# Kernel tuning notes

Measured on AMD Instinct MI355X. Metric: run time of the kernel, lower is better.

The kernel has to match this reference:

```python
import jax, jax.numpy as jnp
import numpy as np

B, C_IN, H, W = 8, 128, 64, 64
C_KEY, C_VAL, C_OUT = 64, 64, 128
BN_EPS = 1e-5
NORM_EPS = 1e-7


def setup_inputs() -> dict:
    key = jax.random.key(0)
    ks = jax.random.split(key, 8)
    s = 0.02
    return {
        "query_feature": jax.random.normal(ks[0], (B, C_IN, H, W), jnp.float32),
        "key_feature": jax.random.normal(ks[1], (B, C_IN, H, W), jnp.float32),
        "value_feature": jax.random.normal(ks[2], (B, C_IN, H, W), jnp.float32),
        "Wk": jax.random.normal(ks[3], (C_KEY, C_IN), jnp.float32) * s,  # shared f_key/f_query 1x1 conv
        "bk": jnp.zeros((C_KEY,), jnp.float32),
        "gamma": jnp.ones((C_KEY,), jnp.float32),   # BatchNorm2d weight
        "beta": jnp.zeros((C_KEY,), jnp.float32),   # BatchNorm2d bias
        "Wv": jax.random.normal(ks[4], (C_VAL, C_IN), jnp.float32) * s,
        "bv": jnp.zeros((C_VAL,), jnp.float32),
        "Ww": jax.random.normal(ks[5], (C_OUT, C_VAL), jnp.float32) * s,  # zero-init in original; random for nontrivial output
        "bw": jnp.zeros((C_OUT,), jnp.float32),
    }


def _conv1x1(x, w, b):
    # x: [B,C,H,W], w: [O,C] -> [B,O,H,W]
    return jnp.einsum('bchw,oc->bohw', x, w) + b[None, :, None, None]


def _bn_train(y, gamma, beta):
    # BatchNorm2d in train mode: batch stats over (B,H,W) per channel
    m = y.mean(axis=(0, 2, 3), keepdims=True)
    v = y.var(axis=(0, 2, 3), keepdims=True)
    return (y - m) * jax.lax.rsqrt(v + BN_EPS) * gamma[None, :, None, None] + beta[None, :, None, None]


def reference(query_feature, key_feature, value_feature, Wk, bk, gamma, beta, Wv, bv, Ww, bw):
    b, _, h, w = query_feature.shape
    n = h * w

    def f_key(x):
        return _bn_train(_conv1x1(x, Wk, bk), gamma, beta)

    # query: [B,N,Ck], key: [B,Ck,N], value: [B,N,Cv]
    q = f_key(query_feature).reshape(b, C_KEY, n).transpose(0, 2, 1)
    k = f_key(key_feature).reshape(b, C_KEY, n)
    v = _conv1x1(value_feature, Wv, bv).reshape(b, C_VAL, n).transpose(0, 2, 1)

    # L2-normalize over channel dim (cosine similarity)
    q = q / (jnp.linalg.norm(q, axis=2, keepdims=True) + NORM_EPS)
    k = k / (jnp.linalg.norm(k, axis=1, keepdims=True) + NORM_EPS)

    sim = jnp.einsum('bnc,bcm->bnm', q, k) + 1.0     # [B,N,N], no softmax
    ctx = jnp.einsum('bnm,bmv->bnv', sim, v)         # [B,N,Cv]
    ctx = ctx.transpose(0, 2, 1).reshape(b, C_VAL, h, w)
    return _conv1x1(ctx, Ww, bw)
```

## Files before the change

### kernel.cpp

```cpp
#include <hip/hip_runtime.h>
#include <math.h>

#define NTOT 4096
#define NBATCH 8
#define CIN 128
#define CK 64
#define CV 64
#define CO 128
#define BN_COUNT 32768.0f

#define OFF_YQ    0ul
#define OFF_YK    2097152ul
#define OFF_V     4194304ul
#define OFF_STATS 6291456ul
#define OFF_M     2097152ul
#define OFF_D     2162688ul
#define KVP_FLOATS   2097152ul
#define VSUMP_OFF    2097152ul

__global__ __launch_bounds__(256) void gemm3_kernel(
    const float* __restrict__ Xq, const float* __restrict__ Xk, const float* __restrict__ Xv,
    const float* __restrict__ Wk, const float* __restrict__ bk,
    const float* __restrict__ Wv, const float* __restrict__ bv,
    float* __restrict__ Yq, float* __restrict__ Yk, float* __restrict__ Vv)
{
    const int chunk = blockIdx.x;
    const int b     = blockIdx.y;
    const int which = blockIdx.z;
    const float* X    = (which == 0) ? Xq : (which == 1) ? Xk : Xv;
    const float* W    = (which == 2) ? Wv : Wk;
    const float* bias = (which == 2) ? bv : bk;
    float* Y          = (which == 0) ? Yq : (which == 1) ? Yk : Vv;

    __shared__ float sX[CIN][64];

    const int t = threadIdx.x;
    const int lane = t & 63;
    const int wu = __builtin_amdgcn_readfirstlane(t >> 6);

    const int n0 = chunk * 64;
    const float* Xb = X + (size_t)b * (CIN * NTOT) + n0;

#pragma unroll
    for (int r = 0; r < 8; ++r) {
        int idx4 = t + r * 256;
        int c  = idx4 >> 4;
        int j4 = (idx4 & 15) << 2;
        float4 xv = *(const float4*)(Xb + (size_t)c * NTOT + j4);
        *(float4*)&sX[c][j4] = xv;
    }
    __syncthreads();

    const float* Wp = W + (size_t)wu * 16 * CIN;
    float acc[16];
#pragma unroll
    for (int ki = 0; ki < 16; ++ki) acc[ki] = 0.f;

#pragma unroll 8
    for (int c = 0; c < CIN; ++c) {
        float xv = sX[c][lane];
#pragma unroll
        for (int ki = 0; ki < 16; ++ki)
            acc[ki] += xv * Wp[ki * CIN + c];
    }

    float* Yb = Y + (size_t)b * (CK * NTOT) + n0;
#pragma unroll
    for (int ki = 0; ki < 16; ++ki) {
        int o = wu * 16 + ki;
        Yb[(size_t)o * NTOT + lane] = acc[ki] + bias[o];
    }
}

__global__ __launch_bounds__(256) void stats_kernel(
    const float* __restrict__ Yq, const float* __restrict__ Yk,
    float* __restrict__ statsP)
{
    const int nsplit = blockIdx.x;
    const int c      = blockIdx.y;
    const int which  = blockIdx.z;
    const float* Y = which ? Yk : Yq;
    const int t = threadIdx.x;

    float s = 0.f, ss = 0.f;
#pragma unroll
    for (int p = 0; p < 4; ++p) {
        int b = (t >> 7) + p * 2;
        int e = (t & 127) << 2;
        const float* src = Y + (size_t)b * (CK * NTOT) + (size_t)c * NTOT
                         + nsplit * 512 + e;
        float4 v = *(const float4*)src;
        s  += v.x + v.y + v.z + v.w;
        ss += v.x * v.x + v.y * v.y + v.z * v.z + v.w * v.w;
    }
#pragma unroll
    for (int off = 32; off > 0; off >>= 1) {
        s  += __shfl_down(s, off, 64);
        ss += __shfl_down(ss, off, 64);
    }
    __shared__ float red[8];
    int wave = t >> 6, lane = t & 63;
    if (lane == 0) { red[wave * 2] = s; red[wave * 2 + 1] = ss; }
    __syncthreads();
    if (t == 0) {
        float S  = red[0] + red[2] + red[4] + red[6];
        float SS = red[1] + red[3] + red[5] + red[7];
        statsP[(which * 64 + c) * 16 + nsplit]     = S;
        statsP[(which * 64 + c) * 16 + 8 + nsplit] = SS;
    }
}

__global__ __launch_bounds__(256) void kv_kernel(
    const float* __restrict__ Yk, const float* __restrict__ Vv,
    const float* __restrict__ statsP, const float* __restrict__ gamma,
    const float* __restrict__ beta, float* __restrict__ KVp,
    float* __restrict__ vsumP)
{
    const int chunk = blockIdx.x;
    const int b     = blockIdx.y;
    __shared__ float sk[64][68];
    __shared__ float sv[64][68];
    __shared__ float pn[4][64];
    __shared__ float rn[64];
    __shared__ float sscl[64], sshf[64];

    const int t = threadIdx.x;
    const int wave = t >> 6, lane = t & 63;
    if (t < 64) {
        const float* sp = statsP + (size_t)(64 + t) * 16;
        float S = 0.f, SS = 0.f;
#pragma unroll
        for (int ns = 0; ns < 8; ++ns) { S += sp[ns]; SS += sp[8 + ns]; }
        float mean = S * (1.f / BN_COUNT);
        float var  = SS * (1.f / BN_COUNT) - mean * mean;
        float scl  = gamma[t] * rsqrtf(var + 1e-5f);
        sscl[t] = scl;
        sshf[t] = beta[t] - mean * scl;
    }
    __syncthreads();

    const int n0 = chunk * 64;
    const float* Ykb = Yk + (size_t)b * (CK * NTOT) + n0;
    const float* Vb  = Vv + (size_t)b * (CK * NTOT) + n0;

#pragma unroll
    for (int r = 0; r < 4; ++r) {
        int idx4 = t + r * 256;
        int c  = idx4 >> 4;
        int j4 = (idx4 & 15) << 2;
        float4 kf = *(const float4*)(Ykb + (size_t)c * NTOT + j4);
        float4 vf = *(const float4*)(Vb  + (size_t)c * NTOT + j4);
        float scl = sscl[c], sh = sshf[c];
        float4 ks = make_float4(kf.x * scl + sh, kf.y * scl + sh,
                                kf.z * scl + sh, kf.w * scl + sh);
        *(float4*)&sk[c][j4] = ks;
        *(float4*)&sv[c][j4] = vf;
    }
    __syncthreads();

    {
        float s = 0.f;
#pragma unroll
        for (int i = 0; i < 16; ++i) { float x = sk[wave * 16 + i][lane]; s += x * x; }
        pn[wave][lane] = s;
    }
    {
        const int v = t >> 2, q = t & 3;
        float s = 0.f;
#pragma unroll
        for (int i = 0; i < 16; ++i) s += sv[v][q * 16 + i];
        s += __shfl_down(s, 2, 64);
        s += __shfl_down(s, 1, 64);
        if (q == 0) vsumP[((size_t)(b * 64 + chunk)) * 64 + v] = s;
    }
    __syncthreads();
    if (t < 64)
        rn[t] = 1.f / (sqrtf(pn[0][t] + pn[1][t] + pn[2][t] + pn[3][t]) + 1e-7f);
    __syncthreads();

    const int tc = t >> 4, tv = t & 15;
    float acc[4][4];
#pragma unroll
    for (int i = 0; i < 4; ++i)
#pragma unroll
        for (int k2 = 0; k2 < 4; ++k2) acc[i][k2] = 0.f;

#pragma unroll 2
    for (int jq = 0; jq < 16; ++jq) {
        float4 rq = *(const float4*)&rn[jq * 4];
        float4 a4[4], b4[4];
#pragma unroll
        for (int i = 0; i < 4; ++i) {
            float4 k4 = *(const float4*)&sk[tc * 4 + i][jq * 4];
            a4[i] = make_float4(k4.x * rq.x, k4.y * rq.y, k4.z * rq.z, k4.w * rq.w);
        }
#pragma unroll
        for (int k2 = 0; k2 < 4; ++k2) b4[k2] = *(const float4*)&sv[tv * 4 + k2][jq * 4];
#pragma unroll
        for (int i = 0; i < 4; ++i)
#pragma unroll
            for (int k2 = 0; k2 < 4; ++k2) {
                acc[i][k2] += a4[i].x * b4[k2].x + a4[i].y * b4[k2].y
                            + a4[i].z * b4[k2].z + a4[i].w * b4[k2].w;
            }
    }

    float* P = KVp + ((size_t)(b * 64 + chunk)) * 4096;
#pragma unroll
    for (int i = 0; i < 4; ++i) {
        float4 st = make_float4(acc[i][0], acc[i][1], acc[i][2], acc[i][3]);
        *(float4*)&P[(tc * 4 + i) * 64 + tv * 4] = st;
    }
}

__global__ __launch_bounds__(256) void m_kernel(
    const float* __restrict__ KVp, const float* __restrict__ vsumP,
    const float* __restrict__ Ww, const float* __restrict__ bw,
    float* __restrict__ M, float* __restrict__ d)
{
    const int slice = blockIdx.x;
    const int b     = blockIdx.y;
    __shared__ float part[256][4];
    __shared__ float sKV[4][68];
    __shared__ float sWw[128][68];
    __shared__ float vsp[4][64];
    __shared__ float svs[64];
    const int t = threadIdx.x;

#pragma unroll
    for (int r = 0; r < 8; ++r) {
        int idx4 = t + r * 256;
        int o  = idx4 >> 4;
        int v4 = (idx4 & 15) << 2;
        *(float4*)&sWw[o][v4] = *(const float4*)(Ww + (size_t)o * 64 + v4);
    }

    if (slice == 0) {
        int prt = t >> 6;
        int v   = t & 63;
        float s = 0.f;
        for (int ch = prt; ch < 64; ch += 4)
            s += vsumP[((size_t)(b * 64 + ch)) * 64 + v];
        vsp[prt][v] = s;
    }

    const int chl = t >> 6;
    const int ci  = (t >> 4) & 3;
    const int v4  = (t & 15) << 2;
    const size_t rowoff = ((size_t)(slice * 4 + ci)) * 64 + v4;
    float4 a4 = make_float4(0.f, 0.f, 0.f, 0.f);
#pragma unroll 4
    for (int it = 0; it < 16; ++it) {
        int ch = it * 4 + chl;
        float4 x = *(const float4*)(KVp + ((size_t)(b * 64 + ch)) * 4096 + rowoff);
        a4.x += x.x; a4.y += x.y; a4.z += x.z; a4.w += x.w;
    }
    *(float4*)&part[t][0] = a4;
    __syncthreads();
    if (t < 64) {
        float4 p0 = *(const float4*)&part[t][0];
        float4 p1 = *(const float4*)&part[t + 64][0];
        float4 p2 = *(const float4*)&part[t + 128][0];
        float4 p3 = *(const float4*)&part[t + 192][0];
        *(float4*)&sKV[(t >> 4) & 3][(t & 15) << 2] =
            make_float4(p0.x + p1.x + p2.x + p3.x, p0.y + p1.y + p2.y + p3.y,
                        p0.z + p1.z + p2.z + p3.z, p0.w + p1.w + p2.w + p3.w);
    }
    if (slice == 0 && t >= 64 && t < 128) {
        int v = t - 64;
        svs[v] = vsp[0][v] + vsp[1][v] + vsp[2][v] + vsp[3][v];
    }
    __syncthreads();

    float* Mb = M + (size_t)b * (CK * CO);
#pragma unroll
    for (int rep = 0; rep < 2; ++rep) {
        int idx = t + rep * 256;
        int c = idx >> 7, o = idx & 127;
        float acc = 0.f;
#pragma unroll
        for (int vq = 0; vq < 16; ++vq) {
            float4 kv4 = *(const float4*)&sKV[c][vq * 4];
            float4 w4  = *(const float4*)&sWw[o][vq * 4];
            acc += kv4.x * w4.x + kv4.y * w4.y + kv4.z * w4.z + kv4.w * w4.w;
        }
        Mb[(size_t)(slice * 4 + c) * CO + o] = acc;
    }

    if (slice == 0 && t < 128) {
        float acc = bw[t];
#pragma unroll 16
        for (int v = 0; v < 64; ++v) acc += sWw[t][v] * svs[v];
        d[(size_t)b * CO + t] = acc;
    }
}

__global__ __launch_bounds__(256) void out_kernel(
    const float* __restrict__ Yq, const float* __restrict__ statsP,
    const float* __restrict__ gamma, const float* __restrict__ beta,
    const float* __restrict__ M, const float* __restrict__ d,
    float* __restrict__ out)
{
    const int chunk = blockIdx.x;
    const int b     = blockIdx.y;
    __shared__ float sM[CK * CO];
    __shared__ float sq[64][36];
    __shared__ float pn[8][32];
    __shared__ float rn[32];
    __shared__ float sd[CO];
    __shared__ float sscl[64], sshf[64];

    const int t = threadIdx.x;
    const int n0 = chunk * 32;

#pragma unroll
    for (int r = 0; r < 8; ++r) {
        int idx4 = t + r * 256;
        ((float4*)sM)[idx4] = ((const float4*)(M + (size_t)b * (CK * CO)))[idx4];
    }
    if (t < CO) sd[t] = d[(size_t)b * CO + t];
    if (t < 64) {
        const float* sp = statsP + (size_t)t * 16;
        float S = 0.f, SS = 0.f;
#pragma unroll
        for (int ns = 0; ns < 8; ++ns) { S += sp[ns]; SS += sp[8 + ns]; }
        float mean = S * (1.f / BN_COUNT);
        float var  = SS * (1.f / BN_COUNT) - mean * mean;
        float scl  = gamma[t] * rsqrtf(var + 1e-5f);
        sscl[t] = scl;
        sshf[t] = beta[t] - mean * scl;
    }
    __syncthreads();

    const float* Yb = Yq + (size_t)b * (CK * NTOT) + n0;
#pragma unroll
    for (int r = 0; r < 2; ++r) {
        int idx4 = t + r * 256;
        int c  = idx4 >> 3;
        int j4 = (idx4 & 7) << 2;
        float4 xv = *(const float4*)(Yb + (size_t)c * NTOT + j4);
        float scl = sscl[c], sh = sshf[c];
        sq[c][j4 + 0] = xv.x * scl + sh;
        sq[c][j4 + 1] = xv.y * scl + sh;
        sq[c][j4 + 2] = xv.z * scl + sh;
        sq[c][j4 + 3] = xv.w * scl + sh;
    }
    __syncthreads();

    {
        const int col = t & 31, g = t >> 5;
        float s = 0.f;
#pragma unroll
        for (int i = 0; i < 8; ++i) { float x = sq[g * 8 + i][col]; s += x * x; }
        pn[g][col] = s;
    }
    __syncthreads();
    if (t < 32) {
        float s2 = pn[0][t] + pn[1][t] + pn[2][t] + pn[3][t]
                 + pn[4][t] + pn[5][t] + pn[6][t] + pn[7][t];
        rn[t] = 1.f / (sqrtf(s2) + 1e-7f);
    }
    __syncthreads();

    const int j0 = (t & 7) << 2;
    const int o0 = (t >> 3) << 2;
    float acc[4][4];
#pragma unroll
    for (int jj = 0; jj < 4; ++jj)
#pragma unroll
        for (int oo = 0; oo < 4; ++oo) acc[jj][oo] = 0.f;

#pragma unroll 4
    for (int c = 0; c < 64; ++c) {
        float4 qv = *(const float4*)&sq[c][j0];
        float4 m0 = *(const float4*)&sM[c * CO + o0];
        float aq[4] = {qv.x, qv.y, qv.z, qv.w};
        float am[4] = {m0.x, m0.y, m0.z, m0.w};
#pragma unroll
        for (int jj = 0; jj < 4; ++jj)
#pragma unroll
            for (int oo = 0; oo < 4; ++oo) acc[jj][oo] += aq[jj] * am[oo];
    }

    float4 rq = *(const float4*)&rn[j0];

    float* outb = out + (size_t)b * (CO * NTOT) + n0;
#pragma unroll
    for (int oo = 0; oo < 4; ++oo) {
        float dd = sd[o0 + oo];
        float4 st = make_float4(acc[0][oo] * rq.x + dd,
                                acc[1][oo] * rq.y + dd,
                                acc[2][oo] * rq.z + dd,
                                acc[3][oo] * rq.w + dd);
        *(float4*)&outb[(size_t)(o0 + oo) * NTOT + j0] = st;
    }
}

extern "C" void kernel_launch(void* const* d_in, const int* in_sizes, int n_in,
                              void* d_out, int out_size, void* d_ws, size_t ws_size,
                              hipStream_t stream) {
    (void)in_sizes; (void)n_in; (void)out_size; (void)ws_size;
    const float* q     = (const float*)d_in[0];
    const float* k     = (const float*)d_in[1];
    const float* v     = (const float*)d_in[2];
    const float* Wk    = (const float*)d_in[3];
    const float* bk    = (const float*)d_in[4];
    const float* gamma = (const float*)d_in[5];
    const float* beta  = (const float*)d_in[6];
    const float* Wv    = (const float*)d_in[7];
    const float* bv    = (const float*)d_in[8];
    const float* Ww    = (const float*)d_in[9];
    const float* bw    = (const float*)d_in[10];
    float* out = (float*)d_out;
    float* ws  = (float*)d_ws;

    float* Yq    = ws + OFF_YQ;
    float* Yk    = ws + OFF_YK;
    float* Vv    = ws + OFF_V;
    float* stats = ws + OFF_STATS;
    float* M     = ws + OFF_M;
    float* dd    = ws + OFF_D;
    float* KVp   = out;
    float* vsumP = out + VSUMP_OFF;

    gemm3_kernel<<<dim3(64, NBATCH, 3), 256, 0, stream>>>(
        q, k, v, Wk, bk, Wv, bv, Yq, Yk, Vv);
    stats_kernel<<<dim3(8, 64, 2), 256, 0, stream>>>(Yq, Yk, stats);
    kv_kernel<<<dim3(64, NBATCH), 256, 0, stream>>>(Yk, Vv, stats, gamma, beta, KVp, vsumP);
    m_kernel<<<dim3(16, NBATCH), 256, 0, stream>>>(KVp, vsumP, Ww, bw, M, dd);
    out_kernel<<<dim3(128, NBATCH), 256, 0, stream>>>(Yq, stats, gamma, beta, M, dd, out);
}
```

Before: 182.7 us.

## Fuse stats, KV, M and output kernels into one persistent kernel with grid barriers

Replaces four separate kernel launches with a single 512-block persistent kernel. Phases are separated by atomic-counter grid barriers, and the counters are reset by the first gemm kernel. This removes launch gaps and inter-kernel drains. The output phase now tiles 64 columns per block with an 8x4 accumulator instead of 32 columns. The risks are deadlock if not all 512 blocks are co-resident (launch bounds request 2 blocks/CU), idle blocks in the M phase, and spin-wait overhead.

```diff
diff --git a/kernel.cpp b/kernel.cpp
--- a/kernel.cpp
+++ b/kernel.cpp
@@ -8,22 +8,39 @@
 #define CV 64
 #define CO 128
 #define BN_COUNT 32768.0f
+#define GRID_N 512u
 
 #define OFF_YQ    0ul
 #define OFF_YK    2097152ul
 #define OFF_V     4194304ul
 #define OFF_STATS 6291456ul
+#define OFF_CTR   6293504ul
 #define OFF_M     2097152ul
 #define OFF_D     2162688ul
-#define KVP_FLOATS   2097152ul
-#define VSUMP_OFF    2097152ul
+#define VSUMP_OFF 2097152ul
+
+__device__ __forceinline__ void grid_barrier(unsigned* c) {
+    __syncthreads();
+    if (threadIdx.x == 0) {
+        __threadfence();
+        __hip_atomic_fetch_add(c, 1u, __ATOMIC_RELEASE, __HIP_MEMORY_SCOPE_AGENT);
+        while (__hip_atomic_load(c, __ATOMIC_ACQUIRE, __HIP_MEMORY_SCOPE_AGENT) < GRID_N)
+            __builtin_amdgcn_s_sleep(2);
+        __threadfence();
+    }
+    __syncthreads();
+}
 
 __global__ __launch_bounds__(256) void gemm3_kernel(
     const float* __restrict__ Xq, const float* __restrict__ Xk, const float* __restrict__ Xv,
     const float* __restrict__ Wk, const float* __restrict__ bk,
     const float* __restrict__ Wv, const float* __restrict__ bv,
-    float* __restrict__ Yq, float* __restrict__ Yk, float* __restrict__ Vv)
+    float* __restrict__ Yq, float* __restrict__ Yk, float* __restrict__ Vv,
+    unsigned* __restrict__ ctr)
 {
+    if (blockIdx.x == 0 && blockIdx.y == 0 && blockIdx.z == 0 && threadIdx.x == 0) {
+        ctr[0] = 0u; ctr[1] = 0u; ctr[2] = 0u;
+    }
     const int chunk = blockIdx.x;
     const int b     = blockIdx.y;
     const int which = blockIdx.z;
@@ -72,327 +89,325 @@
     }
 }
 
-__global__ __launch_bounds__(256) void stats_kernel(
+__global__ __launch_bounds__(256, 2) void fused_kernel(
     const float* __restrict__ Yq, const float* __restrict__ Yk,
-    float* __restrict__ statsP)
+    const float* __restrict__ Vv, float* __restrict__ statsP,
+    const float* __restrict__ gamma, const float* __restrict__ beta,
+    const float* __restrict__ Ww, const float* __restrict__ bw,
+    float* __restrict__ KVp, float* __restrict__ vsumP,
+    float* __restrict__ M, float* __restrict__ d, float* __restrict__ out,
+    unsigned* __restrict__ ctr)
 {
-    const int nsplit = blockIdx.x;
-    const int c      = blockIdx.y;
-    const int which  = blockIdx.z;
-    const float* Y = which ? Yk : Yq;
+    __shared__ __align__(16) char smem[52480];
     const int t = threadIdx.x;
-
-    float s = 0.f, ss = 0.f;
-#pragma unroll
-    for (int p = 0; p < 4; ++p) {
-        int b = (t >> 7) + p * 2;
-        int e = (t & 127) << 2;
-        const float* src = Y + (size_t)b * (CK * NTOT) + (size_t)c * NTOT
-                         + nsplit * 512 + e;
-        float4 v = *(const float4*)src;
-        s  += v.x + v.y + v.z + v.w;
-        ss += v.x * v.x + v.y * v.y + v.z * v.z + v.w * v.w;
-    }
-#pragma unroll
-    for (int off = 32; off > 0; off >>= 1) {
-        s  += __shfl_down(s, off, 64);
-        ss += __shfl_down(ss, off, 64);
-    }
-    __shared__ float red[8];
-    int wave = t >> 6, lane = t & 63;
-    if (lane == 0) { red[wave * 2] = s; red[wave * 2 + 1] = ss; }
-    __syncthreads();
-    if (t == 0) {
-        float S  = red[0] + red[2] + red[4] + red[6];
-        float SS = red[1] + red[3] + red[5] + red[7];
-        statsP[(which * 64 + c) * 16 + nsplit]     = S;
-        statsP[(which * 64 + c) * 16 + 8 + nsplit] = SS;
-    }
-}
-
-__global__ __launch_bounds__(256) void kv_kernel(
-    const float* __restrict__ Yk, const float* __restrict__ Vv,
-    const float* __restrict__ statsP, const float* __restrict__ gamma,
-    const float* __restrict__ beta, float* __restrict__ KVp,
-    float* __restrict__ vsumP)
-{
-    const int chunk = blockIdx.x;
-    const int b     = blockIdx.y;
-    __shared__ float sk[64][68];
-    __shared__ float sv[64][68];
-    __shared__ float pn[4][64];
-    __shared__ float rn[64];
-    __shared__ float sscl[64], sshf[64];
-
-    const int t = threadIdx.x;
+    const int blk = blockIdx.x;
     const int wave = t >> 6, lane = t & 63;
-    if (t < 64) {
-        const float* sp = statsP + (size_t)(64 + t) * 16;
-        float S = 0.f, SS = 0.f;
-#pragma unroll
-        for (int ns = 0; ns < 8; ++ns) { S += sp[ns]; SS += sp[8 + ns]; }
-        float mean = S * (1.f / BN_COUNT);
-        float var  = SS * (1.f / BN_COUNT) - mean * mean;
-        float scl  = gamma[t] * rsqrtf(var + 1e-5f);
-        sscl[t] = scl;
-        sshf[t] = beta[t] - mean * scl;
-    }
-    __syncthreads();
-
-    const int n0 = chunk * 64;
-    const float* Ykb = Yk + (size_t)b * (CK * NTOT) + n0;
-    const float* Vb  = Vv + (size_t)b * (CK * NTOT) + n0;
-
-#pragma unroll
-    for (int r = 0; r < 4; ++r) {
-        int idx4 = t + r * 256;
-        int c  = idx4 >> 4;
-        int j4 = (idx4 & 15) << 2;
-        float4 kf = *(const float4*)(Ykb + (size_t)c * NTOT + j4);
-        float4 vf = *(const float4*)(Vb  + (size_t)c * NTOT + j4);
-        float scl = sscl[c], sh = sshf[c];
-        float4 ks = make_float4(kf.x * scl + sh, kf.y * scl + sh,
-                                kf.z * scl + sh, kf.w * scl + sh);
-        *(float4*)&sk[c][j4] = ks;
-        *(float4*)&sv[c][j4] = vf;
-    }
-    __syncthreads();
 
     {
-        float s = 0.f;
-#pragma unroll
-        for (int i = 0; i < 16; ++i) { float x = sk[wave * 16 + i][lane]; s += x * x; }
-        pn[wave][lane] = s;
-    }
+        float* red = (float*)(void*)smem;
+#pragma unroll
+        for (int rep = 0; rep < 2; ++rep) {
+            int u = blk + rep * 512;
+            int which = u >> 9;
+            int c     = (u >> 3) & 63;
+            int ns    = u & 7;
+            const float* Y = which ? Yk : Yq;
+            float s = 0.f, ss = 0.f;
+#pragma unroll
+            for (int p = 0; p < 4; ++p) {
+                int b = (t >> 7) + p * 2;
+                int e = (t & 127) << 2;
+                const float* src = Y + (size_t)b * (CK * NTOT) + (size_t)c * NTOT
+                                 + ns * 512 + e;
+                float4 v = *(const float4*)src;
+                s  += v.x + v.y + v.z + v.w;
+                ss += v.x * v.x + v.y * v.y + v.z * v.z + v.w * v.w;
+            }
+#pragma unroll
+            for (int off = 32; off > 0; off >>= 1) {
+                s  += __shfl_down(s, off, 64);
+                ss += __shfl_down(ss, off, 64);
+            }
+            __syncthreads();
+            if (lane == 0) { red[wave * 2] = s; red[wave * 2 + 1] = ss; }
+            __syncthreads();
+            if (t == 0) {
+                float S  = red[0] + red[2] + red[4] + red[6];
+                float SS = red[1] + red[3] + red[5] + red[7];
+                statsP[(which * 64 + c) * 16 + ns]     = S;
+                statsP[(which * 64 + c) * 16 + 8 + ns] = SS;
+            }
+        }
+    }
+    grid_barrier(&ctr[0]);
+
     {
-        const int v = t >> 2, q = t & 3;
-        float s = 0.f;
-#pragma unroll
-        for (int i = 0; i < 16; ++i) s += sv[v][q * 16 + i];
-        s += __shfl_down(s, 2, 64);
-        s += __shfl_down(s, 1, 64);
-        if (q == 0) vsumP[((size_t)(b * 64 + chunk)) * 64 + v] = s;
-    }
-    __syncthreads();
-    if (t < 64)
-        rn[t] = 1.f / (sqrtf(pn[0][t] + pn[1][t] + pn[2][t] + pn[3][t]) + 1e-7f);
-    __syncthreads();
-
-    const int tc = t >> 4, tv = t & 15;
-    float acc[4][4];
-#pragma unroll
-    for (int i = 0; i < 4; ++i)
-#pragma unroll
-        for (int k2 = 0; k2 < 4; ++k2) acc[i][k2] = 0.f;
+        float (*sk)[68] = (float(*)[68])(void*)(smem);
+        float (*sv)[68] = (float(*)[68])(void*)(smem + 17408);
+        float (*pn)[64] = (float(*)[64])(void*)(smem + 34816);
+        float* rn   = (float*)(void*)(smem + 35840);
+        float* sscl = (float*)(void*)(smem + 36096);
+        float* sshf = (float*)(void*)(smem + 36352);
+        const int chunk = blk & 63;
+        const int b     = blk >> 6;
+
+        if (t < 64) {
+            const float* sp = statsP + (size_t)(64 + t) * 16;
+            float S = 0.f, SS = 0.f;
+#pragma unroll
+            for (int ns = 0; ns < 8; ++ns) { S += sp[ns]; SS += sp[8 + ns]; }
+            float mean = S * (1.f / BN_COUNT);
+            float var  = SS * (1.f / BN_COUNT) - mean * mean;
+            float scl  = gamma[t] * rsqrtf(var + 1e-5f);
+            sscl[t] = scl;
+            sshf[t] = beta[t] - mean * scl;
+        }
+        __syncthreads();
+
+        const int n0 = chunk * 64;
+        const float* Ykb = Yk + (size_t)b * (CK * NTOT) + n0;
+        const float* Vb  = Vv + (size_t)b * (CK * NTOT) + n0;
+
+#pragma unroll
+        for (int r = 0; r < 4; ++r) {
+            int idx4 = t + r * 256;
+            int c  = idx4 >> 4;
+            int j4 = (idx4 & 15) << 2;
+            float4 kf = *(const float4*)(Ykb + (size_t)c * NTOT + j4);
+            float4 vf = *(const float4*)(Vb  + (size_t)c * NTOT + j4);
+            float scl = sscl[c], sh = sshf[c];
+            float4 ks = make_float4(kf.x * scl + sh, kf.y * scl + sh,
+                                    kf.z * scl + sh, kf.w * scl + sh);
+            *(float4*)&sk[c][j4] = ks;
+            *(float4*)&sv[c][j4] = vf;
+        }
+        __syncthreads();
+
+        {
+            float s = 0.f;
+#pragma unroll
+            for (int i = 0; i < 16; ++i) { float x = sk[wave * 16 + i][lane]; s += x * x; }
+            pn[wave][lane] = s;
+        }
+        {
+            const int v = t >> 2, q = t & 3;
+            float s = 0.f;
+#pragma unroll
+            for (int i = 0; i < 16; ++i) s += sv[v][q * 16 + i];
+            s += __shfl_down(s, 2, 64);
+            s += __shfl_down(s, 1, 64);
+            if (q == 0) vsumP[((size_t)(b * 64 + chunk)) * 64 + v] = s;
+        }
+        __syncthreads();
+        if (t < 64)
+            rn[t] = 1.f / (sqrtf(pn[0][t] + pn[1][t] + pn[2][t] + pn[3][t]) + 1e-7f);
+        __syncthreads();
+
+        const int tc = t >> 4, tv = t & 15;
+        float acc[4][4];
+#pragma unroll
+        for (int i = 0; i < 4; ++i)
+#pragma unroll
+            for (int k2 = 0; k2 < 4; ++k2) acc[i][k2] = 0.f;
 
 #pragma unroll 2
-    for (int jq = 0; jq < 16; ++jq) {
-        float4 rq = *(const float4*)&rn[jq * 4];
-        float4 a4[4], b4[4];
+        for (int jq = 0; jq < 16; ++jq) {
+            float4 rq = *(const float4*)&rn[jq * 4];
+            float4 a4[4], b4[4];
+#pragma unroll
+            for (int i = 0; i < 4; ++i) {
+                float4 k4 = *(const float4*)&sk[tc * 4 + i][jq * 4];
+                a4[i] = make_float4(k4.x * rq.x, k4.y * rq.y, k4.z * rq.z, k4.w * rq.w);
+            }
+#pragma unroll
+            for (int k2 = 0; k2 < 4; ++k2) b4[k2] = *(const float4*)&sv[tv * 4 + k2][jq * 4];
+#pragma unroll
+            for (int i = 0; i < 4; ++i)
+#pragma unroll
+                for (int k2 = 0; k2 < 4; ++k2) {
+                    acc[i][k2] += a4[i].x * b4[k2].x + a4[i].y * b4[k2].y
+                                + a4[i].z * b4[k2].z + a4[i].w * b4[k2].w;
+                }
+        }
+
+        float* P = KVp + ((size_t)(b * 64 + chunk)) * 4096;
 #pragma unroll
         for (int i = 0; i < 4; ++i) {
-            float4 k4 = *(const float4*)&sk[tc * 4 + i][jq * 4];
-            a4[i] = make_float4(k4.x * rq.x, k4.y * rq.y, k4.z * rq.z, k4.w * rq.w);
-        }
-#pragma unroll
-        for (int k2 = 0; k2 < 4; ++k2) b4[k2] = *(const float4*)&sv[tv * 4 + k2][jq * 4];
-#pragma unroll
-        for (int i = 0; i < 4; ++i)
-#pragma unroll
-            for (int k2 = 0; k2 < 4; ++k2) {
-                acc[i][k2] += a4[i].x * b4[k2].x + a4[i].y * b4[k2].y
-                            + a4[i].z * b4[k2].z + a4[i].w * b4[k2].w;
+            float4 st = make_float4(acc[i][0], acc[i][1], acc[i][2], acc[i][3]);
+            *(float4*)&P[(tc * 4 + i) * 64 + tv * 4] = st;
+        }
+    }
+    grid_barrier(&ctr[1]);
+
+    if (blk < 128) {
+        float (*sWw)[68] = (float(*)[68])(void*)(smem);
+        float (*part)[4] = (float(*)[4])(void*)(smem + 34816);
+        float (*sKV)[68] = (float(*)[68])(void*)(smem + 38912);
+        float (*vsp)[64] = (float(*)[64])(void*)(smem + 40000);
+        float* svs = (float*)(void*)(smem + 41024);
+        const int slice = blk & 15;
+        const int b     = blk >> 4;
+
+#pragma unroll
+        for (int r = 0; r < 8; ++r) {
+            int idx4 = t + r * 256;
+            int o  = idx4 >> 4;
+            int v4 = (idx4 & 15) << 2;
+            *(float4*)&sWw[o][v4] = *(const float4*)(Ww + (size_t)o * 64 + v4);
+        }
+
+        if (slice == 0) {
+            int prt = t >> 6;
+            int v   = t & 63;
+            float s = 0.f;
+            for (int ch = prt; ch < 64; ch += 4)
+                s += vsumP[((size_t)(b * 64 + ch)) * 64 + v];
+            vsp[prt][v] = s;
+        }
+
+        const int chl = t >> 6;
+        const int ci  = (t >> 4) & 3;
+        const int v4  = (t & 15) << 2;
+        const size_t rowoff = ((size_t)(slice * 4 + ci)) * 64 + v4;
+        float4 a4 = make_float4(0.f, 0.f, 0.f, 0.f);
+#pragma unroll 4
+        for (int it = 0; it < 16; ++it) {
+            int ch = it * 4 + chl;
+            float4 x = *(const float4*)(KVp + ((size_t)(b * 64 + ch)) * 4096 + rowoff);
+            a4.x += x.x; a4.y += x.y; a4.z += x.z; a4.w += x.w;
+        }
+        *(float4*)&part[t][0] = a4;
+        __syncthreads();
+        if (t < 64) {
+            float4 p0 = *(const float4*)&part[t][0];
+            float4 p1 = *(const float4*)&part[t + 64][0];
+            float4 p2 = *(const float4*)&part[t + 128][0];
+            float4 p3 = *(const float4*)&part[t + 192][0];
+            *(float4*)&sKV[(t >> 4) & 3][(t & 15) << 2] =
+                make_float4(p0.x + p1.x + p2.x + p3.x, p0.y + p1.y + p2.y + p3.y,
+                            p0.z + p1.z + p2.z + p3.z, p0.w + p1.w + p2.w + p3.w);
+        }
+        if (slice == 0 && t >= 64 && t < 128) {
+            int v = t - 64;
+            svs[v] = vsp[0][v] + vsp[1][v] + vsp[2][v] + vsp[3][v];
+        }
+        __syncthreads();
+
+        float* Mb = M + (size_t)b * (CK * CO);
+#pragma unroll
+        for (int rep = 0; rep < 2; ++rep) {
+            int idx = t + rep * 256;
+            int c = idx >> 7, o = idx & 127;
+            float acc = 0.f;
+#pragma unroll
+            for (int vq = 0; vq < 16; ++vq) {
+                float4 kv4 = *(const float4*)&sKV[c][vq * 4];
+                float4 w4  = *(const float4*)&sWw[o][vq * 4];
+                acc += kv4.x * w4.x + kv4.y * w4.y + kv4.z * w4.z + kv4.w * w4.w;
             }
-    }
-
-    float* P = KVp + ((size_t)(b * 64 + chunk)) * 4096;
-#pragma unroll
-    for (int i = 0; i < 4; ++i) {
-        float4 st = make_float4(acc[i][0], acc[i][1], acc[i][2], acc[i][3]);
-        *(float4*)&P[(tc * 4 + i) * 64 + tv * 4] = st;
-    }
-}
-
-__global__ __launch_bounds__(256) void m_kernel(
-    const float* __restrict__ KVp, const float* __restrict__ vsumP,
-    const float* __restrict__ Ww, const float* __restrict__ bw,
-    float* __restrict__ M, float* __restrict__ d)
-{
-    const int slice = blockIdx.x;
-    const int b     = blockIdx.y;
-    __shared__ float part[256][4];
-    __shared__ float sKV[4][68];
-    __shared__ float sWw[128][68];
-    __shared__ float vsp[4][64];
-    __shared__ float svs[64];
-    const int t = threadIdx.x;
-
-#pragma unroll
-    for (int r = 0; r < 8; ++r) {
-        int idx4 = t + r * 256;
-        int o  = idx4 >> 4;
-        int v4 = (idx4 & 15) << 2;
-        *(float4*)&sWw[o][v4] = *(const float4*)(Ww + (size_t)o * 64 + v4);
-    }
-
-    if (slice == 0) {
-        int prt = t >> 6;
-        int v   = t & 63;
-        float s = 0.f;
-        for (int ch = prt; ch < 64; ch += 4)
-            s += vsumP[((size_t)(b * 64 + ch)) * 64 + v];
-        vsp[prt][v] = s;
-    }
-
-    const int chl = t >> 6;
-    const int ci  = (t >> 4) & 3;
-    const int v4  = (t & 15) << 2;
-    const size_t rowoff = ((size_t)(slice * 4 + ci)) * 64 + v4;
-    float4 a4 = make_float4(0.f, 0.f, 0.f, 0.f);
+            Mb[(size_t)(slice * 4 + c) * CO + o] = acc;
+        }
+
+        if (slice == 0 && t < 128) {
+            float acc = bw[t];
+#pragma unroll 16
+            for (int v = 0; v < 64; ++v) acc += sWw[t][v] * svs[v];
+            d[(size_t)b * CO + t] = acc;
+        }
+    }
+    grid_barrier(&ctr[2]);
+
+    {
+        float* sM       = (float*)(void*)(smem);
+        float (*sq)[68] = (float(*)[68])(void*)(smem + 32768);
+        float (*pn)[64] = (float(*)[64])(void*)(smem + 50176);
+        float* rn   = (float*)(void*)(smem + 51200);
+        float* sd   = (float*)(void*)(smem + 51456);
+        float* sscl = (float*)(void*)(smem + 51968);
+        float* sshf = (float*)(void*)(smem + 52224);
+        const int chunk = blk & 63;
+        const int b     = blk >> 6;
+        const int n0 = chunk * 64;
+
+#pragma unroll
+        for (int r = 0; r < 8; ++r) {
+            int idx4 = t + r * 256;
+            ((float4*)sM)[idx4] = ((const float4*)(M + (size_t)b * (CK * CO)))[idx4];
+        }
+        if (t < CO) sd[t] = d[(size_t)b * CO + t];
+        if (t < 64) {
+            const float* sp = statsP + (size_t)t * 16;
+            float S = 0.f, SS = 0.f;
+#pragma unroll
+            for (int ns = 0; ns < 8; ++ns) { S += sp[ns]; SS += sp[8 + ns]; }
+            float mean = S * (1.f / BN_COUNT);
+            float var  = SS * (1.f / BN_COUNT) - mean * mean;
+            float scl  = gamma[t] * rsqrtf(var + 1e-5f);
+            sscl[t] = scl;
+            sshf[t] = beta[t] - mean * scl;
+        }
+        __syncthreads();
+
+        const float* Yb = Yq + (size_t)b * (CK * NTOT) + n0;
+#pragma unroll
+        for (int r = 0; r < 4; ++r) {
+            int idx4 = t + r * 256;
+            int c  = idx4 >> 4;
+            int j4 = (idx4 & 15) << 2;
+            float4 xv = *(const float4*)(Yb + (size_t)c * NTOT + j4);
+            float scl = sscl[c], sh = sshf[c];
+            sq[c][j4 + 0] = xv.x * scl + sh;
+            sq[c][j4 + 1] = xv.y * scl + sh;
+            sq[c][j4 + 2] = xv.z * scl + sh;
+            sq[c][j4 + 3] = xv.w * scl + sh;
+        }
+        __syncthreads();
+
+        {
+            float s = 0.f;
+#pragma unroll
+            for (int i = 0; i < 16; ++i) { float x = sq[wave * 16 + i][lane]; s += x * x; }
+            pn[wave][lane] = s;
+        }
+        __syncthreads();
+        if (t < 64)
+            rn[t] = 1.f / (sqrtf(pn[0][t] + pn[1][t] + pn[2][t] + pn[3][t]) + 1e-7f);
+        __syncthreads();
+
+        const int j0 = (t & 15) << 2;
+        const int o0 = (t >> 4) << 3;
+        float acc[4][8];
+#pragma unroll
+        for (int jj = 0; jj < 4; ++jj)
+#pragma unroll
+            for (int oo = 0; oo < 8; ++oo) acc[jj][oo] = 0.f;
+
 #pragma unroll 4
-    for (int it = 0; it < 16; ++it) {
-        int ch = it * 4 + chl;
-        float4 x = *(const float4*)(KVp + ((size_t)(b * 64 + ch)) * 4096 + rowoff);
-        a4.x += x.x; a4.y += x.y; a4.z += x.z; a4.w += x.w;
-    }
-    *(float4*)&part[t][0] = a4;
-    __syncthreads();
-    if (t < 64) {
-        float4 p0 = *(const float4*)&part[t][0];
-        float4 p1 = *(const float4*)&part[t + 64][0];
-        float4 p2 = *(const float4*)&part[t + 128][0];
-        float4 p3 = *(const float4*)&part[t + 192][0];
-        *(float4*)&sKV[(t >> 4) & 3][(t & 15) << 2] =
-            make_float4(p0.x + p1.x + p2.x + p3.x, p0.y + p1.y + p2.y + p3.y,
-                        p0.z + p1.z + p2.z + p3.z, p0.w + p1.w + p2.w + p3.w);
-    }
-    if (slice == 0 && t >= 64 && t < 128) {
-        int v = t - 64;
-        svs[v] = vsp[0][v] + vsp[1][v] + vsp[2][v] + vsp[3][v];
-    }
-    __syncthreads();
-
-    float* Mb = M + (size_t)b * (CK * CO);
-#pragma unroll
-    for (int rep = 0; rep < 2; ++rep) {
-        int idx = t + rep * 256;
-        int c = idx >> 7, o = idx & 127;
-        float acc = 0.f;
-#pragma unroll
-        for (int vq = 0; vq < 16; ++vq) {
-            float4 kv4 = *(const float4*)&sKV[c][vq * 4];
-            float4 w4  = *(const float4*)&sWw[o][vq * 4];
-            acc += kv4.x * w4.x + kv4.y * w4.y + kv4.z * w4.z + kv4.w * w4.w;
-        }
-        Mb[(size_t)(slice * 4 + c) * CO + o] = acc;
-    }
-
-    if (slice == 0 && t < 128) {
-        float acc = bw[t];
-#pragma unroll 16
-        for (int v = 0; v < 64; ++v) acc += sWw[t][v] * svs[v];
-        d[(size_t)b * CO + t] = acc;
-    }
-}
-
-__global__ __launch_bounds__(256) void out_kernel(
-    const float* __restrict__ Yq, const float* __restrict__ statsP,
-    const float* __restrict__ gamma, const float* __restrict__ beta,
-    const float* __restrict__ M, const float* __restrict__ d,
-    float* __restrict__ out)
-{
-    const int chunk = blockIdx.x;
-    const int b     = blockIdx.y;
-    __shared__ float sM[CK * CO];
-    __shared__ float sq[64][36];
-    __shared__ float pn[8][32];
-    __shared__ float rn[32];
-    __shared__ float sd[CO];
-    __shared__ float sscl[64], sshf[64];
-
-    const int t = threadIdx.x;
-    const int n0 = chunk * 32;
-
-#pragma unroll
-    for (int r = 0; r < 8; ++r) {
-        int idx4 = t + r * 256;
-        ((float4*)sM)[idx4] = ((const float4*)(M + (size_t)b * (CK * CO)))[idx4];
-    }
-    if (t < CO) sd[t] = d[(size_t)b * CO + t];
-    if (t < 64) {
-        const float* sp = statsP + (size_t)t * 16;
-        float S = 0.f, SS = 0.f;
-#pragma unroll
-        for (int ns = 0; ns < 8; ++ns) { S += sp[ns]; SS += sp[8 + ns]; }
-        float mean = S * (1.f / BN_COUNT);
-        float var  = SS * (1.f / BN_COUNT) - mean * mean;
-        float scl  = gamma[t] * rsqrtf(var + 1e-5f);
-        sscl[t] = scl;
-        sshf[t] = beta[t] - mean * scl;
-    }
-    __syncthreads();
-
-    const float* Yb = Yq + (size_t)b * (CK * NTOT) + n0;
-#pragma unroll
-    for (int r = 0; r < 2; ++r) {
-        int idx4 = t + r * 256;
-        int c  = idx4 >> 3;
-        int j4 = (idx4 & 7) << 2;
-        float4 xv = *(const float4*)(Yb + (size_t)c * NTOT + j4);
-        float scl = sscl[c], sh = sshf[c];
-        sq[c][j4 + 0] = xv.x * scl + sh;
-        sq[c][j4 + 1] = xv.y * scl + sh;
-        sq[c][j4 + 2] = xv.z * scl + sh;
-        sq[c][j4 + 3] = xv.w * scl + sh;
-    }
-    __syncthreads();
-
-    {
-        const int col = t & 31, g = t >> 5;
-        float s = 0.f;
-#pragma unroll
-        for (int i = 0; i < 8; ++i) { float x = sq[g * 8 + i][col]; s += x * x; }
-        pn[g][col] = s;
-    }
-    __syncthreads();
-    if (t < 32) {
-        float s2 = pn[0][t] + pn[1][t] + pn[2][t] + pn[3][t]
-                 + pn[4][t] + pn[5][t] + pn[6][t] + pn[7][t];
-        rn[t] = 1.f / (sqrtf(s2) + 1e-7f);
-    }
-    __syncthreads();
-
-    const int j0 = (t & 7) << 2;
-    const int o0 = (t >> 3) << 2;
-    float acc[4][4];
-#pragma unroll
-    for (int jj = 0; jj < 4; ++jj)
-#pragma unroll
-        for (int oo = 0; oo < 4; ++oo) acc[jj][oo] = 0.f;
-
-#pragma unroll 4
-    for (int c = 0; c < 64; ++c) {
-        float4 qv = *(const float4*)&sq[c][j0];
-        float4 m0 = *(const float4*)&sM[c * CO + o0];
-        float aq[4] = {qv.x, qv.y, qv.z, qv.w};
-        float am[4] = {m0.x, m0.y, m0.z, m0.w};
-#pragma unroll
-        for (int jj = 0; jj < 4; ++jj)
-#pragma unroll
-            for (int oo = 0; oo < 4; ++oo) acc[jj][oo] += aq[jj] * am[oo];
-    }
-
-    float4 rq = *(const float4*)&rn[j0];
-
-    float* outb = out + (size_t)b * (CO * NTOT) + n0;
-#pragma unroll
-    for (int oo = 0; oo < 4; ++oo) {
-        float dd = sd[o0 + oo];
-        float4 st = make_float4(acc[0][oo] * rq.x + dd,
-                                acc[1][oo] * rq.y + dd,
-                                acc[2][oo] * rq.z + dd,
-                                acc[3][oo] * rq.w + dd);
-        *(float4*)&outb[(size_t)(o0 + oo) * NTOT + j0] = st;
+        for (int c = 0; c < 64; ++c) {
+            float4 qv = *(const float4*)&sq[c][j0];
+            float4 m0 = *(const float4*)&sM[c * CO + o0];
+            float4 m1 = *(const float4*)&sM[c * CO + o0 + 4];
+            float aq[4] = {qv.x, qv.y, qv.z, qv.w};
+            float am[8] = {m0.x, m0.y, m0.z, m0.w, m1.x, m1.y, m1.z, m1.w};
+#pragma unroll
+            for (int jj = 0; jj < 4; ++jj)
+#pragma unroll
+                for (int oo = 0; oo < 8; ++oo) acc[jj][oo] += aq[jj] * am[oo];
+        }
+
+        float4 rq = *(const float4*)&rn[j0];
+        float rnj[4] = {rq.x, rq.y, rq.z, rq.w};
+
+        float* outb = out + (size_t)b * (CO * NTOT) + n0;
+#pragma unroll
+        for (int oo = 0; oo < 8; ++oo) {
+            float dd = sd[o0 + oo];
+            float4 st = make_float4(acc[0][oo] * rnj[0] + dd,
+                                    acc[1][oo] * rnj[1] + dd,
+                                    acc[2][oo] * rnj[2] + dd,
+                                    acc[3][oo] * rnj[3] + dd);
+            *(float4*)&outb[(size_t)(o0 + oo) * NTOT + j0] = st;
+        }
     }
 }
 
@@ -418,15 +433,15 @@
     float* Yk    = ws + OFF_YK;
     float* Vv    = ws + OFF_V;
     float* stats = ws + OFF_STATS;
+    unsigned* ctr = (unsigned*)(ws + OFF_CTR);
     float* M     = ws + OFF_M;
     float* dd    = ws + OFF_D;
     float* KVp   = out;
     float* vsumP = out + VSUMP_OFF;
 
     gemm3_kernel<<<dim3(64, NBATCH, 3), 256, 0, stream>>>(
-        q, k, v, Wk, bk, Wv, bv, Yq, Yk, Vv);
-    stats_kernel<<<dim3(8, 64, 2), 256, 0, stream>>>(Yq, Yk, stats);
-    kv_kernel<<<dim3(64, NBATCH), 256, 0, stream>>>(Yk, Vv, stats, gamma, beta, KVp, vsumP);
-    m_kernel<<<dim3(16, NBATCH), 256, 0, stream>>>(KVp, vsumP, Ww, bw, M, dd);
-    out_kernel<<<dim3(128, NBATCH), 256, 0, stream>>>(Yq, stats, gamma, beta, M, dd, out);
+        q, k, v, Wk, bk, Wv, bv, Yq, Yk, Vv, ctr);
+
+    fused_kernel<<<dim3(GRID_N), 256, 0, stream>>>(
+        Yq, Yk, Vv, stats, gamma, beta, Ww, bw, KVp, vsumP, M, dd, out, ctr);
 }
```

After: 359.7 us. 96.9% more time.
